# Kernel optimization log

Measured on AMD Instinct MI355X. Metric: run time of the kernel, lower is better.

The kernel has to match this reference:

```python
import jax, jax.numpy as jnp
import numpy as np

WS = 8        # window_size
NH = 12       # num_heads


def setup_inputs() -> dict:
    key = jax.random.key(0)
    ks = jax.random.split(key, 9)
    B, C, H, W = 4, 384, 128, 128
    s = 1.0 / np.sqrt(C)
    x = jax.random.normal(ks[0], (B, C, H, W), dtype=jnp.float32)
    Wq = jax.random.normal(ks[1], (C, C), dtype=jnp.float32) * s
    bq = jax.random.normal(ks[2], (C,), dtype=jnp.float32) * 0.01
    Wk = jax.random.normal(ks[3], (C, C), dtype=jnp.float32) * s
    bk = jax.random.normal(ks[4], (C,), dtype=jnp.float32) * 0.01
    Wv = jax.random.normal(ks[5], (C, C), dtype=jnp.float32) * s
    bv = jax.random.normal(ks[6], (C,), dtype=jnp.float32) * 0.01
    Wp = jax.random.normal(ks[7], (C, C), dtype=jnp.float32) * s
    bp = jax.random.normal(ks[8], (C,), dtype=jnp.float32) * 0.01
    return {"x": x, "Wq": Wq, "bq": bq, "Wk": Wk, "bk": bk,
            "Wv": Wv, "bv": bv, "Wp": Wp, "bp": bp}


def reference(x, Wq, bq, Wk, bk, Wv, bv, Wp, bp):
    B, C, H, W = x.shape
    ws2 = WS * WS
    dk = C // NH
    scale = dk ** -0.5

    # window_partition: flat row-major reshape (same semantics as torch's
    # reshape on a contiguous [B,C,H,W] tensor), then permute+view.
    p = x.reshape(B, H // WS, WS, W // WS, WS, C)
    p = jnp.transpose(p, (0, 5, 1, 3, 2, 4))          # [B, C, H/ws, W/ws, ws, ws]
    p = p.reshape(B, C, -1, ws2)                       # [B, C, nW, ws*ws]

    def conv1x1(w, b):  # 1x1 Conv2d on [B,C,nW,ws2]
        return jnp.einsum('bcnw,oc->bonw', p, w) + b[None, :, None, None]

    def heads(t):  # permute(0,2,3,1).contiguous().reshape -> [B, NH, nW, ws2, dk]
        t = jnp.transpose(t, (0, 2, 3, 1))             # [B, nW, ws2, C]
        return t.reshape(B, NH, -1, ws2, dk)           # row-major reinterpretation

    q = heads(conv1x1(Wq, bq))
    k = heads(conv1x1(Wk, bk))
    v = heads(conv1x1(Wv, bv))

    scores = jnp.einsum('bhnqd,bhnkd->bhnqk', q, k) * scale
    attn = jax.nn.softmax(scores, axis=-1)
    o = jnp.einsum('bhnqk,bhnkd->bhnqd', attn, v)      # [B, NH, nW, ws2, dk]
    o = o.reshape(B, -1, ws2, C)                       # [B, nW, ws2, C]

    # window_unpartition
    u = o.reshape(B, -1, WS, WS, C)
    u = jnp.transpose(u, (0, 4, 1, 2, 3))              # [B, C, nW, ws, ws]
    u = u.reshape(B, C, H, W)

    y = jnp.einsum('bchw,oc->bohw', u, Wp) + bp[None, :, None, None]
    return y
```

## Files before the change

kernel.cpp:

```cpp
#include <hip/hip_runtime.h>
#include <hip/hip_bf16.h>
#include <stdint.h>


typedef __bf16 bf16_t;
typedef __bf16 bf16x8 __attribute__((ext_vector_type(8)));
typedef __bf16 bf16x4 __attribute__((ext_vector_type(4)));
typedef float f32x4 __attribute__((ext_vector_type(4)));

__device__ __forceinline__ void gload_lds16(const void* g, void* l) {
  __builtin_amdgcn_global_load_lds((__attribute__((address_space(1))) void*)(g),
                                   (__attribute__((address_space(3))) void*)(l),
                                   16, 0, 0);
}

__global__ __launch_bounds__(256) void convw_kernel(
    const float* __restrict__ wq, const float* __restrict__ wk,
    const float* __restrict__ wv, const float* __restrict__ wp,
    bf16_t* __restrict__ oq, bf16_t* __restrict__ ok,
    bf16_t* __restrict__ ov, bf16_t* __restrict__ op_) {
  int i = blockIdx.x * 256 + threadIdx.x;
  oq[i] = (bf16_t)wq[i];
  ok[i] = (bf16_t)wk[i];
  ov[i] = (bf16_t)wv[i];
  op_[i] = (bf16_t)wp[i];
}

__global__ __launch_bounds__(256) void prep_kernel(const float* __restrict__ x,
                                                   bf16_t* __restrict__ Xp) {
  int gid = blockIdx.x * 256 + threadIdx.x;
  int row = gid / 96;
  int c4 = (gid - row * 96) * 4;
  int b = row >> 14;
  int pp = row & 16383;
  int n1 = pp >> 10, n3 = (pp >> 6) & 15, w2 = (pp >> 3) & 7, w4 = pp & 7;
  int P = (n1 << 10) | (w2 << 7) | (n3 << 3) | w4;
  float4 v = *(const float4*)(x + (size_t)((b << 14) | P) * 384 + c4);
  bf16x4 o;
  o[0] = (bf16_t)v.x; o[1] = (bf16_t)v.y; o[2] = (bf16_t)v.z; o[3] = (bf16_t)v.w;
  *(bf16x4*)(Xp + (size_t)row * 384 + c4) = o;
}

__device__ __forceinline__ void stage_tile(const bf16_t* __restrict__ A,
                                           const bf16_t* __restrict__ B,
                                           bf16_t* As, bf16_t* Bs, int k0, int tid) {
  const int lane = tid & 63, wv = tid >> 6;
#pragma unroll
  for (int j = 0; j < 2; ++j) {
    int q = wv * 128 + j * 64 + lane;
    int row = q >> 2, c16 = q & 3;
    gload_lds16(A + (size_t)row * 384 + k0 + c16 * 8,
                (char*)As + (wv * 128 + j * 64) * 16);
    gload_lds16(B + (size_t)row * 384 + k0 + c16 * 8,
                (char*)Bs + (wv * 128 + j * 64) * 16);
  }
}

__device__ __forceinline__ void gemm_mainloop(const bf16_t* __restrict__ Arows,
                                              const bf16_t* __restrict__ Brows,
                                              bf16_t* As, bf16_t* Bs,
                                              int tid, f32x4 acc[4][4]) {
  const int lane = tid & 63;
  const int l15 = lane & 15, hi = lane >> 4;
  const int wr = (tid >> 6) >> 1, wc = (tid >> 6) & 1;
  stage_tile(Arows, Brows, As, Bs, 0, tid);
  stage_tile(Arows, Brows, As + 4096, Bs + 4096, 32, tid);
#pragma unroll
  for (int kt = 0; kt < 12; ++kt) {
    bf16_t* Ab = As + (kt & 1) * 4096;
    bf16_t* Bb = Bs + (kt & 1) * 4096;
    if (kt == 11) asm volatile("s_waitcnt vmcnt(0)" ::: "memory");
    else          asm volatile("s_waitcnt vmcnt(4)" ::: "memory");
    __builtin_amdgcn_s_barrier();
    bf16x8 a[4], b[4];
#pragma unroll
    for (int i = 0; i < 4; ++i) {
      a[i] = *(const bf16x8*)(Ab + (wr * 64 + i * 16 + l15) * 32 + hi * 8);
      b[i] = *(const bf16x8*)(Bb + (wc * 64 + i * 16 + l15) * 32 + hi * 8);
    }
#pragma unroll
    for (int mi = 0; mi < 4; ++mi)
#pragma unroll
      for (int ni = 0; ni < 4; ++ni)
        acc[mi][ni] = __builtin_amdgcn_mfma_f32_16x16x32_bf16(a[mi], b[ni],
                                                              acc[mi][ni], 0, 0, 0);
    asm volatile("s_waitcnt lgkmcnt(0)" ::: "memory");
    __builtin_amdgcn_sched_barrier(0);
    __builtin_amdgcn_s_barrier();
    if (kt + 2 < 12)
      stage_tile(Arows, Brows, Ab, Bb, (kt + 2) * 32, tid);
  }
}

__global__ __launch_bounds__(256) void qkv_gemm(
    const bf16_t* __restrict__ Xp, const bf16_t* __restrict__ Wcat,
    const float* __restrict__ bq, const float* __restrict__ bk,
    const float* __restrict__ bv,
    bf16_t* __restrict__ Qs, bf16_t* __restrict__ Ks, bf16_t* __restrict__ Vs) {
  __shared__ __align__(16) bf16_t As[2 * 128 * 32];
  __shared__ __align__(16) bf16_t Bs[2 * 128 * 32];
  const int tid = threadIdx.x;
  const int F = blockIdx.x;
  const int xcd = F & 7;
  const int t = F >> 3;
  const int j = t % 9;
  const int gq = t / 9;
  const int m0 = (gq * 8 + xcd) * 128;
  const int which = j / 3;
  const int cb = (j % 3) * 128;
  const float* bias = which == 0 ? bq : (which == 1 ? bk : bv);
  bf16_t* Out = which == 0 ? Qs : (which == 1 ? Ks : Vs);
  f32x4 acc[4][4] = {};
  gemm_mainloop(Xp + (size_t)m0 * 384, Wcat + (size_t)j * 128 * 384,
                As, Bs, tid, acc);
  const int lane = tid & 63, wv = tid >> 6;
  const int l15 = lane & 15, hi = lane >> 4;
  const int wr = wv >> 1, wc = wv & 1;
#pragma unroll
  for (int ni = 0; ni < 4; ++ni) {
    int chan = cb + wc * 64 + ni * 16 + l15;
    float bv_ = bias[chan];
#pragma unroll
    for (int mi = 0; mi < 4; ++mi)
#pragma unroll
      for (int r = 0; r < 4; ++r) {
        int row = m0 + wr * 64 + mi * 16 + hi * 4 + r;
        Out[(size_t)row * 384 + chan] = (bf16_t)(acc[mi][ni][r] + bv_);
      }
  }
}

__global__ __launch_bounds__(64) void attn_kernel(const bf16_t* __restrict__ Q,
                                                  const bf16_t* __restrict__ K,
                                                  const bf16_t* __restrict__ V,
                                                  bf16_t* __restrict__ O) {
  const size_t base = (size_t)blockIdx.x * 2048;
  const bf16_t* q = Q + base;
  const bf16_t* k = K + base;
  const bf16_t* v = V + base;
  bf16_t* o = O + base;
  const int lane = threadIdx.x;
  const int l15 = lane & 15, hi = lane >> 4;

  __shared__ __align__(16) bf16_t Vt[32][72];
  __shared__ __align__(16) bf16_t Ps[64][72];

#pragma unroll
  for (int j = 0; j < 4; ++j) {
    bf16x8 vv = *(const bf16x8*)(v + lane * 32 + j * 8);
#pragma unroll
    for (int e = 0; e < 8; ++e) Vt[j * 8 + e][lane] = vv[e];
  }

  bf16x8 aQ[4], bK[4];
#pragma unroll
  for (int i = 0; i < 4; ++i) {
    aQ[i] = *(const bf16x8*)(q + (i * 16 + l15) * 32 + hi * 8);
    bK[i] = *(const bf16x8*)(k + (i * 16 + l15) * 32 + hi * 8);
  }
  f32x4 sc[4][4] = {};
#pragma unroll
  for (int mi = 0; mi < 4; ++mi)
#pragma unroll
    for (int ni = 0; ni < 4; ++ni)
      sc[mi][ni] = __builtin_amdgcn_mfma_f32_16x16x32_bf16(aQ[mi], bK[ni],
                                                           sc[mi][ni], 0, 0, 0);

  const float SCALE = 0.17677669529663687f;
  float rs[4][4];
#pragma unroll
  for (int mi = 0; mi < 4; ++mi) {
#pragma unroll
    for (int r = 0; r < 4; ++r) {
      float s0 = sc[mi][0][r] * SCALE, s1 = sc[mi][1][r] * SCALE;
      float s2 = sc[mi][2][r] * SCALE, s3 = sc[mi][3][r] * SCALE;
      float mx = fmaxf(fmaxf(s0, s1), fmaxf(s2, s3));
      mx = fmaxf(mx, __shfl_xor(mx, 1));
      mx = fmaxf(mx, __shfl_xor(mx, 2));
      mx = fmaxf(mx, __shfl_xor(mx, 4));
      mx = fmaxf(mx, __shfl_xor(mx, 8));
      float p0 = __expf(s0 - mx), p1 = __expf(s1 - mx);
      float p2 = __expf(s2 - mx), p3 = __expf(s3 - mx);
      int row = mi * 16 + hi * 4 + r;
      Ps[row][0 + l15] = (bf16_t)p0;
      Ps[row][16 + l15] = (bf16_t)p1;
      Ps[row][32 + l15] = (bf16_t)p2;
      Ps[row][48 + l15] = (bf16_t)p3;
      float sum = p0 + p1 + p2 + p3;
      sum += __shfl_xor(sum, 1);
      sum += __shfl_xor(sum, 2);
      sum += __shfl_xor(sum, 4);
      sum += __shfl_xor(sum, 8);
      rs[mi][r] = sum;
    }
  }
  __syncthreads();

  f32x4 oacc[4][2] = {};
#pragma unroll
  for (int mi = 0; mi < 4; ++mi)
#pragma unroll
    for (int ks = 0; ks < 2; ++ks) {
      bf16x8 aP = *(const bf16x8*)(&Ps[mi * 16 + l15][ks * 32 + hi * 8]);
#pragma unroll
      for (int n2 = 0; n2 < 2; ++n2) {
        bf16x8 bV = *(const bf16x8*)(&Vt[n2 * 16 + l15][ks * 32 + hi * 8]);
        oacc[mi][n2] = __builtin_amdgcn_mfma_f32_16x16x32_bf16(aP, bV,
                                                               oacc[mi][n2], 0, 0, 0);
      }
    }
#pragma unroll
  for (int mi = 0; mi < 4; ++mi)
#pragma unroll
    for (int n2 = 0; n2 < 2; ++n2)
#pragma unroll
      for (int r = 0; r < 4; ++r) {
        int row = mi * 16 + hi * 4 + r;
        o[row * 32 + n2 * 16 + l15] = (bf16_t)(oacc[mi][n2][r] / rs[mi][r]);
      }
}

__global__ __launch_bounds__(256) void proj_gemm(const bf16_t* __restrict__ Wpb,
                                                 const bf16_t* __restrict__ O,
                                                 const float* __restrict__ bp,
                                                 float* __restrict__ y) {
  __shared__ __align__(16) bf16_t As[2 * 128 * 32];
  __shared__ __align__(16) bf16_t Bs[2 * 128 * 32];
  const int tid = threadIdx.x;
  const int F = blockIdx.x;
  const int xcd = F & 7;
  const int t = F >> 3;
  const int j = t % 3;
  const int gq = t / 3;
  const int g = gq * 8 + xcd;
  const int n0 = (g & 127) * 128;
  const int b = g >> 7;
  const int m0 = j * 128;
  f32x4 acc[4][4] = {};
  gemm_mainloop(Wpb + (size_t)m0 * 384, O + ((size_t)b * 16384 + n0) * 384,
                As, Bs, tid, acc);
  const int lane = tid & 63, wv = tid >> 6;
  const int l15 = lane & 15, hi = lane >> 4;
  const int wr = wv >> 1, wc = wv & 1;
  float* yb = y + (size_t)b * 6291456;
#pragma unroll
  for (int mi = 0; mi < 4; ++mi)
#pragma unroll
    for (int r = 0; r < 4; ++r) {
      int och = m0 + wr * 64 + mi * 16 + hi * 4 + r;
      float bpv = bp[och];
#pragma unroll
      for (int ni = 0; ni < 4; ++ni) {
        int pix = n0 + wc * 64 + ni * 16 + l15;
        yb[(size_t)och * 16384 + pix] = acc[mi][ni][r] + bpv;
      }
    }
}

extern "C" void kernel_launch(void* const* d_in, const int* in_sizes, int n_in,
                              void* d_out, int out_size, void* d_ws, size_t ws_size,
                              hipStream_t stream) {
  const float* x  = (const float*)d_in[0];
  const float* Wq = (const float*)d_in[1];
  const float* bq = (const float*)d_in[2];
  const float* Wk = (const float*)d_in[3];
  const float* bk = (const float*)d_in[4];
  const float* Wv = (const float*)d_in[5];
  const float* bv = (const float*)d_in[6];
  const float* Wp = (const float*)d_in[7];
  const float* bp = (const float*)d_in[8];
  float* y = (float*)d_out;

  char* ws = (char*)d_ws;
  const size_t SZ = 50331648;
  bf16_t* Xp  = (bf16_t*)(ws);
  bf16_t* Vs  = (bf16_t*)(ws + SZ);
  bf16_t* Wcat = (bf16_t*)(ws + 2 * SZ);
  bf16_t* Wkb = Wcat + 147456;
  bf16_t* Wvb = Wkb + 147456;
  bf16_t* Wpb = Wvb + 147456;
  bf16_t* Qs  = (bf16_t*)d_out;
  bf16_t* Ks  = (bf16_t*)((char*)d_out + SZ);
  bf16_t* Ob  = Xp;

  convw_kernel<<<576, 256, 0, stream>>>(Wq, Wk, Wv, Wp, Wcat, Wkb, Wvb, Wpb);
  prep_kernel<<<24576, 256, 0, stream>>>(x, Xp);
  qkv_gemm<<<4608, 256, 0, stream>>>(Xp, Wcat, bq, bk, bv, Qs, Ks, Vs);
  attn_kernel<<<12288, 64, 0, stream>>>(Qs, Ks, Vs, Ob);
  proj_gemm<<<1536, 256, 0, stream>>>(Wpb, Ob, bp, y);
}
```

Baseline: 194.3 us.

## Fuse fp32 input permute and bf16 cast into QKV GEMM A-tile loading

Removes the separate prep kernel that permuted and cast x to bf16. The QKV GEMM now loads fp32 rows of x into registers, converts them and writes them into an XOR-swizzled LDS tile, with register double buffering. LDS reads and B staging are also swizzled in both GEMMs to reduce bank conflicts. The QKV epilogue stages output through LDS for coalesced 16-byte stores. The trade-off is that x is re-read in fp32 by three column blocks (twice the bytes of bf16) and register pressure rises.

```diff
diff --git a/kernel.cpp b/kernel.cpp
--- a/kernel.cpp
+++ b/kernel.cpp
@@ -5,7 +5,6 @@
 
 typedef __bf16 bf16_t;
 typedef __bf16 bf16x8 __attribute__((ext_vector_type(8)));
-typedef __bf16 bf16x4 __attribute__((ext_vector_type(4)));
 typedef float f32x4 __attribute__((ext_vector_type(4)));
 
 __device__ __forceinline__ void gload_lds16(const void* g, void* l) {
@@ -26,79 +25,52 @@
   op_[i] = (bf16_t)wp[i];
 }
 
-__global__ __launch_bounds__(256) void prep_kernel(const float* __restrict__ x,
-                                                   bf16_t* __restrict__ Xp) {
-  int gid = blockIdx.x * 256 + threadIdx.x;
-  int row = gid / 96;
-  int c4 = (gid - row * 96) * 4;
-  int b = row >> 14;
-  int pp = row & 16383;
-  int n1 = pp >> 10, n3 = (pp >> 6) & 15, w2 = (pp >> 3) & 7, w4 = pp & 7;
-  int P = (n1 << 10) | (w2 << 7) | (n3 << 3) | w4;
-  float4 v = *(const float4*)(x + (size_t)((b << 14) | P) * 384 + c4);
-  bf16x4 o;
-  o[0] = (bf16_t)v.x; o[1] = (bf16_t)v.y; o[2] = (bf16_t)v.z; o[3] = (bf16_t)v.w;
-  *(bf16x4*)(Xp + (size_t)row * 384 + c4) = o;
-}
-
-__device__ __forceinline__ void stage_tile(const bf16_t* __restrict__ A,
-                                           const bf16_t* __restrict__ B,
-                                           bf16_t* As, bf16_t* Bs, int k0, int tid) {
-  const int lane = tid & 63, wv = tid >> 6;
+__device__ __forceinline__ void stageB(const bf16_t* __restrict__ B,
+                                       bf16_t* Bs, int k0, int tid) {
+  const int lane = tid & 63, wvv = tid >> 6;
+  const int s = (lane & 3) ^ ((lane >> 3) & 3);
 #pragma unroll
   for (int j = 0; j < 2; ++j) {
-    int q = wv * 128 + j * 64 + lane;
-    int row = q >> 2, c16 = q & 3;
-    gload_lds16(A + (size_t)row * 384 + k0 + c16 * 8,
-                (char*)As + (wv * 128 + j * 64) * 16);
-    gload_lds16(B + (size_t)row * 384 + k0 + c16 * 8,
-                (char*)Bs + (wv * 128 + j * 64) * 16);
-  }
-}
-
-__device__ __forceinline__ void gemm_mainloop(const bf16_t* __restrict__ Arows,
-                                              const bf16_t* __restrict__ Brows,
-                                              bf16_t* As, bf16_t* Bs,
-                                              int tid, f32x4 acc[4][4]) {
-  const int lane = tid & 63;
-  const int l15 = lane & 15, hi = lane >> 4;
-  const int wr = (tid >> 6) >> 1, wc = (tid >> 6) & 1;
-  stage_tile(Arows, Brows, As, Bs, 0, tid);
-  stage_tile(Arows, Brows, As + 4096, Bs + 4096, 32, tid);
-#pragma unroll
-  for (int kt = 0; kt < 12; ++kt) {
-    bf16_t* Ab = As + (kt & 1) * 4096;
-    bf16_t* Bb = Bs + (kt & 1) * 4096;
-    if (kt == 11) asm volatile("s_waitcnt vmcnt(0)" ::: "memory");
-    else          asm volatile("s_waitcnt vmcnt(4)" ::: "memory");
-    __builtin_amdgcn_s_barrier();
-    bf16x8 a[4], b[4];
-#pragma unroll
-    for (int i = 0; i < 4; ++i) {
-      a[i] = *(const bf16x8*)(Ab + (wr * 64 + i * 16 + l15) * 32 + hi * 8);
-      b[i] = *(const bf16x8*)(Bb + (wc * 64 + i * 16 + l15) * 32 + hi * 8);
-    }
-#pragma unroll
-    for (int mi = 0; mi < 4; ++mi)
-#pragma unroll
-      for (int ni = 0; ni < 4; ++ni)
-        acc[mi][ni] = __builtin_amdgcn_mfma_f32_16x16x32_bf16(a[mi], b[ni],
-                                                              acc[mi][ni], 0, 0, 0);
-    asm volatile("s_waitcnt lgkmcnt(0)" ::: "memory");
-    __builtin_amdgcn_sched_barrier(0);
-    __builtin_amdgcn_s_barrier();
-    if (kt + 2 < 12)
-      stage_tile(Arows, Brows, Ab, Bb, (kt + 2) * 32, tid);
-  }
+    int q = wvv * 128 + j * 64 + lane;
+    int row = q >> 2;
+    gload_lds16(B + (size_t)row * 384 + k0 + s * 8,
+                (char*)Bs + (wvv * 128 + j * 64) * 16);
+  }
+}
+
+struct ARegs { float4 v0, v1, v2, v3; };
+
+__device__ __forceinline__ ARegs issueA(const float* __restrict__ xr0,
+                                        const float* __restrict__ xr1, int k0) {
+  ARegs a;
+  a.v0 = *(const float4*)(xr0 + k0);
+  a.v1 = *(const float4*)(xr0 + k0 + 4);
+  a.v2 = *(const float4*)(xr1 + k0);
+  a.v3 = *(const float4*)(xr1 + k0 + 4);
+  return a;
+}
+
+__device__ __forceinline__ void writeA(const ARegs& a, bf16_t* Ab,
+                                       int r0loc, int ssw) {
+  bf16x8 p0, p1;
+  p0[0] = (bf16_t)a.v0.x; p0[1] = (bf16_t)a.v0.y;
+  p0[2] = (bf16_t)a.v0.z; p0[3] = (bf16_t)a.v0.w;
+  p0[4] = (bf16_t)a.v1.x; p0[5] = (bf16_t)a.v1.y;
+  p0[6] = (bf16_t)a.v1.z; p0[7] = (bf16_t)a.v1.w;
+  p1[0] = (bf16_t)a.v2.x; p1[1] = (bf16_t)a.v2.y;
+  p1[2] = (bf16_t)a.v2.z; p1[3] = (bf16_t)a.v2.w;
+  p1[4] = (bf16_t)a.v3.x; p1[5] = (bf16_t)a.v3.y;
+  p1[6] = (bf16_t)a.v3.z; p1[7] = (bf16_t)a.v3.w;
+  *(bf16x8*)(Ab + r0loc * 32 + ssw * 8) = p0;
+  *(bf16x8*)(Ab + (r0loc + 16) * 32 + ssw * 8) = p1;
 }
 
 __global__ __launch_bounds__(256) void qkv_gemm(
-    const bf16_t* __restrict__ Xp, const bf16_t* __restrict__ Wcat,
+    const float* __restrict__ x, const bf16_t* __restrict__ Wcat,
     const float* __restrict__ bq, const float* __restrict__ bk,
     const float* __restrict__ bv,
     bf16_t* __restrict__ Qs, bf16_t* __restrict__ Ks, bf16_t* __restrict__ Vs) {
-  __shared__ __align__(16) bf16_t As[2 * 128 * 32];
-  __shared__ __align__(16) bf16_t Bs[2 * 128 * 32];
+  __shared__ __align__(16) bf16_t L[16384];
   const int tid = threadIdx.x;
   const int F = blockIdx.x;
   const int xcd = F & 7;
@@ -110,23 +82,135 @@
   const int cb = (j % 3) * 128;
   const float* bias = which == 0 ? bq : (which == 1 ? bk : bv);
   bf16_t* Out = which == 0 ? Qs : (which == 1 ? Ks : Vs);
+  const bf16_t* Wrows = Wcat + (size_t)j * 128 * 384;
+
+  const int lane = tid & 63, wvv = tid >> 6;
+  const int l15 = lane & 15, hi = lane >> 4;
+  const int wr = wvv >> 1, wc = wvv & 1;
+  const int slot = hi ^ ((l15 >> 1) & 3);
+  const int r0loc = wvv * 32 + (lane >> 2);
+  const int ssw = (lane & 3) ^ ((lane >> 3) & 3);
+
+  const int b = m0 >> 14;
+  const int pp0 = m0 & 16383;
+  auto prow = [&](int pp) {
+    int n1 = pp >> 10, n3 = (pp >> 6) & 15, w2 = (pp >> 3) & 7, w4 = pp & 7;
+    return (size_t)((b << 14) | (n1 << 10) | (w2 << 7) | (n3 << 3) | w4) * 384;
+  };
+  const float* xr0 = x + prow(pp0 + r0loc) + (lane & 3) * 8;
+  const float* xr1 = x + prow(pp0 + r0loc + 16) + (lane & 3) * 8;
+
+  ARegs st0 = issueA(xr0, xr1, 0);
+  stageB(Wrows, L + 4096, 0, tid);
+  ARegs st1 = issueA(xr0, xr1, 32);
+  stageB(Wrows, L + 8192 + 4096, 32, tid);
+
   f32x4 acc[4][4] = {};
-  gemm_mainloop(Xp + (size_t)m0 * 384, Wcat + (size_t)j * 128 * 384,
-                As, Bs, tid, acc);
-  const int lane = tid & 63, wv = tid >> 6;
+#pragma unroll
+  for (int kt = 0; kt < 12; ++kt) {
+    bf16_t* Ab = L + (kt & 1) * 8192;
+    bf16_t* Bb = Ab + 4096;
+    if (kt == 11) asm volatile("s_waitcnt vmcnt(0)" ::: "memory");
+    else          asm volatile("s_waitcnt vmcnt(6)" ::: "memory");
+    __builtin_amdgcn_sched_barrier(0);
+    writeA((kt & 1) ? st1 : st0, Ab, r0loc, ssw);
+    asm volatile("s_waitcnt lgkmcnt(0)" ::: "memory");
+    __builtin_amdgcn_sched_barrier(0);
+    __builtin_amdgcn_s_barrier();
+    bf16x8 a[4], bfr[4];
+#pragma unroll
+    for (int i = 0; i < 4; ++i) {
+      a[i] = *(const bf16x8*)(Ab + (wr * 64 + i * 16 + l15) * 32 + slot * 8);
+      bfr[i] = *(const bf16x8*)(Bb + (wc * 64 + i * 16 + l15) * 32 + slot * 8);
+    }
+#pragma unroll
+    for (int mi = 0; mi < 4; ++mi)
+#pragma unroll
+      for (int ni = 0; ni < 4; ++ni)
+        acc[mi][ni] = __builtin_amdgcn_mfma_f32_16x16x32_bf16(a[mi], bfr[ni],
+                                                              acc[mi][ni], 0, 0, 0);
+    asm volatile("s_waitcnt lgkmcnt(0)" ::: "memory");
+    __builtin_amdgcn_sched_barrier(0);
+    __builtin_amdgcn_s_barrier();
+    if (kt + 2 < 12) {
+      if (kt & 1) st1 = issueA(xr0, xr1, (kt + 2) * 32);
+      else        st0 = issueA(xr0, xr1, (kt + 2) * 32);
+      stageB(Wrows, Bb, (kt + 2) * 32, tid);
+    }
+  }
+
+#pragma unroll
+  for (int ni = 0; ni < 4; ++ni) {
+    int ch = wc * 64 + ni * 16 + l15;
+    float bv_ = bias[cb + ch];
+#pragma unroll
+    for (int mi = 0; mi < 4; ++mi)
+#pragma unroll
+      for (int r = 0; r < 4; ++r) {
+        int row = wr * 64 + mi * 16 + hi * 4 + r;
+        L[row * 128 + ch] = (bf16_t)(acc[mi][ni][r] + bv_);
+      }
+  }
+  __syncthreads();
+#pragma unroll
+  for (int p = 0; p < 8; ++p) {
+    int row = p * 16 + (tid >> 4);
+    int ch = (tid & 15) * 8;
+    bf16x8 val = *(const bf16x8*)(L + row * 128 + ch);
+    *(bf16x8*)(Out + (size_t)(m0 + row) * 384 + cb + ch) = val;
+  }
+}
+
+__device__ __forceinline__ void stage_tile(const bf16_t* __restrict__ A,
+                                           const bf16_t* __restrict__ B,
+                                           bf16_t* As, bf16_t* Bs, int k0, int tid) {
+  const int lane = tid & 63, wvv = tid >> 6;
+  const int s = (lane & 3) ^ ((lane >> 3) & 3);
+#pragma unroll
+  for (int j = 0; j < 2; ++j) {
+    int q = wvv * 128 + j * 64 + lane;
+    int row = q >> 2;
+    gload_lds16(A + (size_t)row * 384 + k0 + s * 8,
+                (char*)As + (wvv * 128 + j * 64) * 16);
+    gload_lds16(B + (size_t)row * 384 + k0 + s * 8,
+                (char*)Bs + (wvv * 128 + j * 64) * 16);
+  }
+}
+
+__device__ __forceinline__ void gemm_mainloop(const bf16_t* __restrict__ Arows,
+                                              const bf16_t* __restrict__ Brows,
+                                              bf16_t* As, bf16_t* Bs,
+                                              int tid, f32x4 acc[4][4]) {
+  const int lane = tid & 63;
   const int l15 = lane & 15, hi = lane >> 4;
-  const int wr = wv >> 1, wc = wv & 1;
-#pragma unroll
-  for (int ni = 0; ni < 4; ++ni) {
-    int chan = cb + wc * 64 + ni * 16 + l15;
-    float bv_ = bias[chan];
+  const int wr = (tid >> 6) >> 1, wc = (tid >> 6) & 1;
+  const int slot = hi ^ ((l15 >> 1) & 3);
+  stage_tile(Arows, Brows, As, Bs, 0, tid);
+  stage_tile(Arows, Brows, As + 4096, Bs + 4096, 32, tid);
+#pragma unroll
+  for (int kt = 0; kt < 12; ++kt) {
+    bf16_t* Ab = As + (kt & 1) * 4096;
+    bf16_t* Bb = Bs + (kt & 1) * 4096;
+    if (kt == 11) asm volatile("s_waitcnt vmcnt(0)" ::: "memory");
+    else          asm volatile("s_waitcnt vmcnt(4)" ::: "memory");
+    __builtin_amdgcn_s_barrier();
+    bf16x8 a[4], bfr[4];
+#pragma unroll
+    for (int i = 0; i < 4; ++i) {
+      a[i] = *(const bf16x8*)(Ab + (wr * 64 + i * 16 + l15) * 32 + slot * 8);
+      bfr[i] = *(const bf16x8*)(Bb + (wc * 64 + i * 16 + l15) * 32 + slot * 8);
+    }
 #pragma unroll
     for (int mi = 0; mi < 4; ++mi)
 #pragma unroll
-      for (int r = 0; r < 4; ++r) {
-        int row = m0 + wr * 64 + mi * 16 + hi * 4 + r;
-        Out[(size_t)row * 384 + chan] = (bf16_t)(acc[mi][ni][r] + bv_);
-      }
+      for (int ni = 0; ni < 4; ++ni)
+        acc[mi][ni] = __builtin_amdgcn_mfma_f32_16x16x32_bf16(a[mi], bfr[ni],
+                                                              acc[mi][ni], 0, 0, 0);
+    asm volatile("s_waitcnt lgkmcnt(0)" ::: "memory");
+    __builtin_amdgcn_sched_barrier(0);
+    __builtin_amdgcn_s_barrier();
+    if (kt + 2 < 12)
+      stage_tile(Arows, Brows, Ab, Bb, (kt + 2) * 32, tid);
   }
 }
 
@@ -239,9 +323,9 @@
   f32x4 acc[4][4] = {};
   gemm_mainloop(Wpb + (size_t)m0 * 384, O + ((size_t)b * 16384 + n0) * 384,
                 As, Bs, tid, acc);
-  const int lane = tid & 63, wv = tid >> 6;
+  const int lane = tid & 63, wvv = tid >> 6;
   const int l15 = lane & 15, hi = lane >> 4;
-  const int wr = wv >> 1, wc = wv & 1;
+  const int wr = wvv >> 1, wc = wvv & 1;
   float* yb = y + (size_t)b * 6291456;
 #pragma unroll
   for (int mi = 0; mi < 4; ++mi)
@@ -273,7 +357,7 @@
 
   char* ws = (char*)d_ws;
   const size_t SZ = 50331648;
-  bf16_t* Xp  = (bf16_t*)(ws);
+  bf16_t* Ob  = (bf16_t*)(ws);
   bf16_t* Vs  = (bf16_t*)(ws + SZ);
   bf16_t* Wcat = (bf16_t*)(ws + 2 * SZ);
   bf16_t* Wkb = Wcat + 147456;
@@ -281,11 +365,9 @@
   bf16_t* Wpb = Wvb + 147456;
   bf16_t* Qs  = (bf16_t*)d_out;
   bf16_t* Ks  = (bf16_t*)((char*)d_out + SZ);
-  bf16_t* Ob  = Xp;
 
   convw_kernel<<<576, 256, 0, stream>>>(Wq, Wk, Wv, Wp, Wcat, Wkb, Wvb, Wpb);
-  prep_kernel<<<24576, 256, 0, stream>>>(x, Xp);
-  qkv_gemm<<<4608, 256, 0, stream>>>(Xp, Wcat, bq, bk, bv, Qs, Ks, Vs);
+  qkv_gemm<<<4608, 256, 0, stream>>>(x, Wcat, bq, bk, bv, Qs, Ks, Vs);
   attn_kernel<<<12288, 64, 0, stream>>>(Qs, Ks, Vs, Ob);
   proj_gemm<<<1536, 256, 0, stream>>>(Wpb, Ob, bp, y);
 }
```

After: 203.3 us. 1.05x slower.

## Enlarge QKV GEMM M-tile to 256 and XOR-swizzle LDS tiles

Applied to the files above, without the earlier changes.

The QKV GEMM now computes a 256x128 output tile per block instead of 128x128. Each wave holds 8x4 accumulator fragments and the grid is halved, so every weight tile loaded is reused across twice as many rows. Both GEMMs also XOR-swizzle the 16-byte chunk placement when staging into LDS and read back with a matching swizzled slot, to reduce LDS bank conflicts. The cost is higher register pressure from 128 accumulator floats per lane, more LDS per block, a non-unrolled k-loop in the QKV kernel, and fewer blocks to fill the GPU.

```diff
diff --git a/kernel.cpp b/kernel.cpp
--- a/kernel.cpp
+++ b/kernel.cpp
@@ -41,63 +41,12 @@
   *(bf16x4*)(Xp + (size_t)row * 384 + c4) = o;
 }
 
-__device__ __forceinline__ void stage_tile(const bf16_t* __restrict__ A,
-                                           const bf16_t* __restrict__ B,
-                                           bf16_t* As, bf16_t* Bs, int k0, int tid) {
-  const int lane = tid & 63, wv = tid >> 6;
-#pragma unroll
-  for (int j = 0; j < 2; ++j) {
-    int q = wv * 128 + j * 64 + lane;
-    int row = q >> 2, c16 = q & 3;
-    gload_lds16(A + (size_t)row * 384 + k0 + c16 * 8,
-                (char*)As + (wv * 128 + j * 64) * 16);
-    gload_lds16(B + (size_t)row * 384 + k0 + c16 * 8,
-                (char*)Bs + (wv * 128 + j * 64) * 16);
-  }
-}
-
-__device__ __forceinline__ void gemm_mainloop(const bf16_t* __restrict__ Arows,
-                                              const bf16_t* __restrict__ Brows,
-                                              bf16_t* As, bf16_t* Bs,
-                                              int tid, f32x4 acc[4][4]) {
-  const int lane = tid & 63;
-  const int l15 = lane & 15, hi = lane >> 4;
-  const int wr = (tid >> 6) >> 1, wc = (tid >> 6) & 1;
-  stage_tile(Arows, Brows, As, Bs, 0, tid);
-  stage_tile(Arows, Brows, As + 4096, Bs + 4096, 32, tid);
-#pragma unroll
-  for (int kt = 0; kt < 12; ++kt) {
-    bf16_t* Ab = As + (kt & 1) * 4096;
-    bf16_t* Bb = Bs + (kt & 1) * 4096;
-    if (kt == 11) asm volatile("s_waitcnt vmcnt(0)" ::: "memory");
-    else          asm volatile("s_waitcnt vmcnt(4)" ::: "memory");
-    __builtin_amdgcn_s_barrier();
-    bf16x8 a[4], b[4];
-#pragma unroll
-    for (int i = 0; i < 4; ++i) {
-      a[i] = *(const bf16x8*)(Ab + (wr * 64 + i * 16 + l15) * 32 + hi * 8);
-      b[i] = *(const bf16x8*)(Bb + (wc * 64 + i * 16 + l15) * 32 + hi * 8);
-    }
-#pragma unroll
-    for (int mi = 0; mi < 4; ++mi)
-#pragma unroll
-      for (int ni = 0; ni < 4; ++ni)
-        acc[mi][ni] = __builtin_amdgcn_mfma_f32_16x16x32_bf16(a[mi], b[ni],
-                                                              acc[mi][ni], 0, 0, 0);
-    asm volatile("s_waitcnt lgkmcnt(0)" ::: "memory");
-    __builtin_amdgcn_sched_barrier(0);
-    __builtin_amdgcn_s_barrier();
-    if (kt + 2 < 12)
-      stage_tile(Arows, Brows, Ab, Bb, (kt + 2) * 32, tid);
-  }
-}
-
 __global__ __launch_bounds__(256) void qkv_gemm(
     const bf16_t* __restrict__ Xp, const bf16_t* __restrict__ Wcat,
     const float* __restrict__ bq, const float* __restrict__ bk,
     const float* __restrict__ bv,
     bf16_t* __restrict__ Qs, bf16_t* __restrict__ Ks, bf16_t* __restrict__ Vs) {
-  __shared__ __align__(16) bf16_t As[2 * 128 * 32];
+  __shared__ __align__(16) bf16_t As[2 * 256 * 32];
   __shared__ __align__(16) bf16_t Bs[2 * 128 * 32];
   const int tid = threadIdx.x;
   const int F = blockIdx.x;
@@ -105,26 +54,80 @@
   const int t = F >> 3;
   const int j = t % 9;
   const int gq = t / 9;
-  const int m0 = (gq * 8 + xcd) * 128;
+  const int m0 = (gq * 8 + xcd) * 256;
   const int which = j / 3;
   const int cb = (j % 3) * 128;
   const float* bias = which == 0 ? bq : (which == 1 ? bk : bv);
   bf16_t* Out = which == 0 ? Qs : (which == 1 ? Ks : Vs);
-  f32x4 acc[4][4] = {};
-  gemm_mainloop(Xp + (size_t)m0 * 384, Wcat + (size_t)j * 128 * 384,
-                As, Bs, tid, acc);
-  const int lane = tid & 63, wv = tid >> 6;
+  const bf16_t* Arows = Xp + (size_t)m0 * 384;
+  const bf16_t* Brows = Wcat + (size_t)j * 128 * 384;
+
+  const int lane = tid & 63, wvv = tid >> 6;
   const int l15 = lane & 15, hi = lane >> 4;
-  const int wr = wv >> 1, wc = wv & 1;
+  const int wrM = wvv >> 1, wc = wvv & 1;
+  const int slot = hi ^ ((l15 >> 1) & 3);
+
+  auto stage = [&](int kt) {
+    const int k0 = kt * 32;
+    bf16_t* Ad = As + (kt & 1) * 8192;
+    bf16_t* Bd = Bs + (kt & 1) * 4096;
+#pragma unroll
+    for (int jj = 0; jj < 4; ++jj) {
+      int idx = jj * 256 + tid;
+      int row = idx >> 2;
+      int sg = (idx & 3) ^ ((idx >> 3) & 3);
+      gload_lds16(Arows + (size_t)row * 384 + k0 + sg * 8,
+                  (char*)Ad + (jj * 256 + wvv * 64) * 16);
+    }
+#pragma unroll
+    for (int h = 0; h < 2; ++h) {
+      int q = wvv * 128 + h * 64 + lane;
+      int row = q >> 2;
+      int sg = (lane & 3) ^ ((lane >> 3) & 3);
+      gload_lds16(Brows + (size_t)row * 384 + k0 + sg * 8,
+                  (char*)Bd + (wvv * 128 + h * 64) * 16);
+    }
+  };
+
+  stage(0);
+  stage(1);
+
+  f32x4 acc[8][4] = {};
+#pragma unroll 1
+  for (int kt = 0; kt < 12; ++kt) {
+    bf16_t* Ab = As + (kt & 1) * 8192;
+    bf16_t* Bb = Bs + (kt & 1) * 4096;
+    if (kt == 11) asm volatile("s_waitcnt vmcnt(0)" ::: "memory");
+    else          asm volatile("s_waitcnt vmcnt(6)" ::: "memory");
+    __builtin_amdgcn_s_barrier();
+    bf16x8 a[8], bfr[4];
+#pragma unroll
+    for (int i = 0; i < 8; ++i)
+      a[i] = *(const bf16x8*)(Ab + (wrM * 128 + i * 16 + l15) * 32 + slot * 8);
+#pragma unroll
+    for (int ni = 0; ni < 4; ++ni)
+      bfr[ni] = *(const bf16x8*)(Bb + (wc * 64 + ni * 16 + l15) * 32 + slot * 8);
+#pragma unroll
+    for (int mi = 0; mi < 8; ++mi)
+#pragma unroll
+      for (int ni = 0; ni < 4; ++ni)
+        acc[mi][ni] = __builtin_amdgcn_mfma_f32_16x16x32_bf16(a[mi], bfr[ni],
+                                                              acc[mi][ni], 0, 0, 0);
+    asm volatile("s_waitcnt lgkmcnt(0)" ::: "memory");
+    __builtin_amdgcn_sched_barrier(0);
+    __builtin_amdgcn_s_barrier();
+    if (kt + 2 < 12) stage(kt + 2);
+  }
+
 #pragma unroll
   for (int ni = 0; ni < 4; ++ni) {
     int chan = cb + wc * 64 + ni * 16 + l15;
     float bv_ = bias[chan];
 #pragma unroll
-    for (int mi = 0; mi < 4; ++mi)
+    for (int mi = 0; mi < 8; ++mi)
 #pragma unroll
       for (int r = 0; r < 4; ++r) {
-        int row = m0 + wr * 64 + mi * 16 + hi * 4 + r;
+        int row = m0 + wrM * 128 + mi * 16 + hi * 4 + r;
         Out[(size_t)row * 384 + chan] = (bf16_t)(acc[mi][ni][r] + bv_);
       }
   }
@@ -220,6 +223,59 @@
       }
 }
 
+__device__ __forceinline__ void stage_tile(const bf16_t* __restrict__ A,
+                                           const bf16_t* __restrict__ B,
+                                           bf16_t* As, bf16_t* Bs, int k0, int tid) {
+  const int lane = tid & 63, wvv = tid >> 6;
+  const int s = (lane & 3) ^ ((lane >> 3) & 3);
+#pragma unroll
+  for (int j = 0; j < 2; ++j) {
+    int q = wvv * 128 + j * 64 + lane;
+    int row = q >> 2;
+    gload_lds16(A + (size_t)row * 384 + k0 + s * 8,
+                (char*)As + (wvv * 128 + j * 64) * 16);
+    gload_lds16(B + (size_t)row * 384 + k0 + s * 8,
+                (char*)Bs + (wvv * 128 + j * 64) * 16);
+  }
+}
+
+__device__ __forceinline__ void gemm_mainloop(const bf16_t* __restrict__ Arows,
+                                              const bf16_t* __restrict__ Brows,
+                                              bf16_t* As, bf16_t* Bs,
+                                              int tid, f32x4 acc[4][4]) {
+  const int lane = tid & 63;
+  const int l15 = lane & 15, hi = lane >> 4;
+  const int wr = (tid >> 6) >> 1, wc = (tid >> 6) & 1;
+  const int slot = hi ^ ((l15 >> 1) & 3);
+  stage_tile(Arows, Brows, As, Bs, 0, tid);
+  stage_tile(Arows, Brows, As + 4096, Bs + 4096, 32, tid);
+#pragma unroll
+  for (int kt = 0; kt < 12; ++kt) {
+    bf16_t* Ab = As + (kt & 1) * 4096;
+    bf16_t* Bb = Bs + (kt & 1) * 4096;
+    if (kt == 11) asm volatile("s_waitcnt vmcnt(0)" ::: "memory");
+    else          asm volatile("s_waitcnt vmcnt(4)" ::: "memory");
+    __builtin_amdgcn_s_barrier();
+    bf16x8 a[4], bfr[4];
+#pragma unroll
+    for (int i = 0; i < 4; ++i) {
+      a[i] = *(const bf16x8*)(Ab + (wr * 64 + i * 16 + l15) * 32 + slot * 8);
+      bfr[i] = *(const bf16x8*)(Bb + (wc * 64 + i * 16 + l15) * 32 + slot * 8);
+    }
+#pragma unroll
+    for (int mi = 0; mi < 4; ++mi)
+#pragma unroll
+      for (int ni = 0; ni < 4; ++ni)
+        acc[mi][ni] = __builtin_amdgcn_mfma_f32_16x16x32_bf16(a[mi], bfr[ni],
+                                                              acc[mi][ni], 0, 0, 0);
+    asm volatile("s_waitcnt lgkmcnt(0)" ::: "memory");
+    __builtin_amdgcn_sched_barrier(0);
+    __builtin_amdgcn_s_barrier();
+    if (kt + 2 < 12)
+      stage_tile(Arows, Brows, Ab, Bb, (kt + 2) * 32, tid);
+  }
+}
+
 __global__ __launch_bounds__(256) void proj_gemm(const bf16_t* __restrict__ Wpb,
                                                  const bf16_t* __restrict__ O,
                                                  const float* __restrict__ bp,
@@ -239,9 +295,9 @@
   f32x4 acc[4][4] = {};
   gemm_mainloop(Wpb + (size_t)m0 * 384, O + ((size_t)b * 16384 + n0) * 384,
                 As, Bs, tid, acc);
-  const int lane = tid & 63, wv = tid >> 6;
+  const int lane = tid & 63, wvv = tid >> 6;
   const int l15 = lane & 15, hi = lane >> 4;
-  const int wr = wv >> 1, wc = wv & 1;
+  const int wr = wvv >> 1, wc = wvv & 1;
   float* yb = y + (size_t)b * 6291456;
 #pragma unroll
   for (int mi = 0; mi < 4; ++mi)
@@ -285,7 +341,7 @@
 
   convw_kernel<<<576, 256, 0, stream>>>(Wq, Wk, Wv, Wp, Wcat, Wkb, Wvb, Wpb);
   prep_kernel<<<24576, 256, 0, stream>>>(x, Xp);
-  qkv_gemm<<<4608, 256, 0, stream>>>(Xp, Wcat, bq, bk, bv, Qs, Ks, Vs);
+  qkv_gemm<<<2304, 256, 0, stream>>>(Xp, Wcat, bq, bk, bv, Qs, Ks, Vs);
   attn_kernel<<<12288, 64, 0, stream>>>(Qs, Ks, Vs, Ob);
   proj_gemm<<<1536, 256, 0, stream>>>(Wpb, Ob, bp, y);
 }
```

Result: slower. 223.4 us (+15.0%).
